# Kernel tuning notes

Hardware: AMD Instinct MI355X
Metric: run time of the kernel (lower is better)

## Reference

```python
import jax, jax.numpy as jnp
import numpy as np

N = 10000
IN_DIM = 512
OUT_DIM = 128
E = 262144


def setup_inputs() -> dict:
    key = jax.random.key(0)
    ks = jax.random.split(key, 7)
    x = jax.random.normal(ks[0], (N, IN_DIM), dtype=jnp.float32)
    adj = jax.random.uniform(ks[1], (N, N), dtype=jnp.float32) * (1.0 / N)
    # xavier-ish scaled params
    weight = jax.random.normal(ks[2], (IN_DIM, OUT_DIM), dtype=jnp.float32) * (1.0 / np.sqrt(IN_DIM))
    weight_two = jax.random.normal(ks[3], (2 * OUT_DIM, OUT_DIM), dtype=jnp.float32) * (1.0 / np.sqrt(2 * OUT_DIM))
    weight_three = jax.random.normal(ks[4], (2 * OUT_DIM, 1), dtype=jnp.float32) * (1.0 / np.sqrt(2 * OUT_DIM))
    train_edges = jax.random.randint(ks[5], (E, 2), 0, N, dtype=jnp.int32)
    train_false_edges = jax.random.randint(ks[6], (E, 2), 0, N, dtype=jnp.int32)
    return {
        "x": x,
        "adj": adj,
        "weight": weight,
        "weight_two": weight_two,
        "weight_three": weight_three,
        "train_edges": train_edges,
        "train_false_edges": train_false_edges,
    }


def reference(x, adj, weight, weight_two, weight_three, train_edges, train_false_edges):
    # encode: z = adj @ (x @ W)   -> [N, OUT_DIM]
    z = adj @ (x @ weight)
    # decode: vectorized per-edge gather of both endpoints
    edges = jnp.concatenate([train_edges, train_false_edges], axis=0)  # [2E, 2]
    zi = z[edges[:, 0]]  # [2E, OUT_DIM]
    zj = z[edges[:, 1]]  # [2E, OUT_DIM]
    z_pair = jnp.concatenate([zi, zj], axis=1)          # [2E, 2*OUT_DIM]
    z_mult = zi * zj                                     # [2E, OUT_DIM]
    z_pair = jax.nn.relu(z_pair) @ weight_two            # [2E, OUT_DIM]
    logits = jnp.concatenate([z_pair, z_mult], axis=1) @ weight_three  # [2E, 1]
    return jax.nn.sigmoid(logits)
```

## Files before the change

kernel.cpp:

```cpp
#include <hip/hip_runtime.h>

#define N_NODES 10000
#define IN_DIM  512
#define OUT_DIM 128
#define NE      262144
#define K_DIM   10000
#define HT_S    10048

#define BM 128
#define BN 128
#define BK 64
#define SPLITS 8
#define KSTEPS_TOTAL 157
#define STEPS_PER_SPLIT 20

typedef __attribute__((ext_vector_type(8))) __bf16 bf16x8;
typedef __attribute__((ext_vector_type(4))) float  f32x4;

__device__ inline ushort f2bf(float f) {
    uint u = __float_as_uint(f);
    return (ushort)((u + 0x7fffu + ((u >> 16) & 1u)) >> 16);
}
__device__ inline float bf2f(ushort s) {
    return __uint_as_float(((uint)s) << 16);
}

__device__ __forceinline__ void gl2lds16(const void* g, void* l) {
    __builtin_amdgcn_global_load_lds(
        (const __attribute__((address_space(1))) void*)g,
        (__attribute__((address_space(3))) void*)l, 16, 0, 0);
}

__global__ __launch_bounds__(256) void k_prep(const float* __restrict__ w,
                                              const float* __restrict__ w2,
                                              const float* __restrict__ w3,
                                              ushort* __restrict__ WT,
                                              float* __restrict__ v,
                                              ushort* __restrict__ hT) {
    const int t = threadIdx.x;
    for (int idx = blockIdx.x * 256 + t; idx < IN_DIM * OUT_DIM; idx += gridDim.x * 256) {
        int k = idx >> 7, n = idx & 127;
        WT[n * IN_DIM + k] = f2bf(w[idx]);
    }
    if (blockIdx.x == 0) {
        float s = 0.f;
        for (int j = 0; j < OUT_DIM; ++j) s += w2[t * OUT_DIM + j] * w3[j];
        v[t] = s;
    }
    if (blockIdx.x == 1) {
        for (int idx = t; idx < 128 * (HT_S - N_NODES); idx += 256) {
            int c = idx / (HT_S - N_NODES), r = idx % (HT_S - N_NODES);
            hT[(size_t)c * HT_S + N_NODES + r] = 0;
        }
    }
}

__global__ __launch_bounds__(64) void k_xw(const float* __restrict__ x,
                                           const ushort* __restrict__ WT,
                                           ushort* __restrict__ hT) {
    const int lane = threadIdx.x;
    const int lr = lane & 15, lg = lane >> 4;
    const int r0 = blockIdx.x * 16;
    const int c0 = blockIdx.y * 32;
    const float* pA = x + (size_t)(r0 + lr) * IN_DIM;

    f32x4 acc[2];
#pragma unroll
    for (int nf = 0; nf < 2; ++nf) acc[nf] = (f32x4){0.f, 0.f, 0.f, 0.f};

#pragma unroll
    for (int st = 0; st < 8; ++st) {
        const int k0 = st * 64;
        bf16x8 abf[2];
#pragma unroll
        for (int kh = 0; kh < 2; ++kh) {
            float4 a0 = *(const float4*)(pA + k0 + kh * 32 + lg * 8);
            float4 a1 = *(const float4*)(pA + k0 + kh * 32 + lg * 8 + 4);
            ushort* ap = (ushort*)&abf[kh];
            ap[0] = f2bf(a0.x); ap[1] = f2bf(a0.y); ap[2] = f2bf(a0.z); ap[3] = f2bf(a0.w);
            ap[4] = f2bf(a1.x); ap[5] = f2bf(a1.y); ap[6] = f2bf(a1.z); ap[7] = f2bf(a1.w);
        }
#pragma unroll
        for (int kh = 0; kh < 2; ++kh)
#pragma unroll
            for (int nf = 0; nf < 2; ++nf) {
                bf16x8 bfv = *(const bf16x8*)(WT + (size_t)(c0 + nf * 16 + lr) * IN_DIM + k0 + kh * 32 + lg * 8);
                acc[nf] = __builtin_amdgcn_mfma_f32_16x16x32_bf16(abf[kh], bfv, acc[nf], 0, 0, 0);
            }
    }

    const int m0 = r0 + lg * 4;
#pragma unroll
    for (int nf = 0; nf < 2; ++nf) {
        int c = c0 + nf * 16 + lr;
        ushort4 pk;
        pk.x = f2bf(acc[nf][0]); pk.y = f2bf(acc[nf][1]);
        pk.z = f2bf(acc[nf][2]); pk.w = f2bf(acc[nf][3]);
        *(ushort4*)(hT + (size_t)c * HT_S + m0) = pk;
    }
}

__global__ __launch_bounds__(256, 3) void k_adj(const float* __restrict__ adj,
                                                const ushort* __restrict__ hT,
                                                float* __restrict__ zp) {
    __shared__ ushort Bs[BN * BK];

    const int tid = threadIdx.x, wave = tid >> 6, lane = tid & 63;
    const int lr = lane & 15, lg = lane >> 4;
    const int m0 = blockIdx.x * BM;
    const int split = blockIdx.y;
    const int step0 = split * STEPS_PER_SPLIT;
    const int step1 = min(step0 + STEPS_PER_SPLIT, KSTEPS_TOTAL);

    long  bbase[4];
    char* bldst[4];
#pragma unroll
    for (int q = 0; q < 4; ++q) {
        int c = tid + q * 256;
        int row = c >> 3, ch = c & 7;
        bbase[q] = (long)row * HT_S + (long)((ch ^ (row & 7)) * 8);
        bldst[q] = (char*)Bs + c * 16;
    }

    const int ar0 = min(m0 + wave * 32 + lr,      N_NODES - 1);
    const int ar1 = min(m0 + wave * 32 + 16 + lr, N_NODES - 1);
    const float* pA0 = adj + (size_t)ar0 * K_DIM;
    const float* pA1 = adj + (size_t)ar1 * K_DIM;

    f32x4 acc[2][8];
#pragma unroll
    for (int mf = 0; mf < 2; ++mf)
#pragma unroll
        for (int nf = 0; nf < 8; ++nf) acc[mf][nf] = (f32x4){0.f, 0.f, 0.f, 0.f};

    const char* Bb = (const char*)Bs;

    for (int st = step0; st < step1; ++st) {
        const int k0 = st * BK;

#pragma unroll
        for (int q = 0; q < 4; ++q)
            gl2lds16(hT + (bbase[q] + k0), bldst[q]);

        float4 fa[2][2][2];
#pragma unroll
        for (int kh = 0; kh < 2; ++kh) {
            int kk = k0 + kh * 32 + lg * 8;
            int kc = (kk <= K_DIM - 8) ? kk : (K_DIM - 8);
            fa[0][kh][0] = *(const float4*)(pA0 + kc);
            fa[0][kh][1] = *(const float4*)(pA0 + kc + 4);
            fa[1][kh][0] = *(const float4*)(pA1 + kc);
            fa[1][kh][1] = *(const float4*)(pA1 + kc + 4);
        }

        __syncthreads();

        bf16x8 abf[2][2];
#pragma unroll
        for (int mf = 0; mf < 2; ++mf)
#pragma unroll
            for (int kh = 0; kh < 2; ++kh) {
                ushort* ap = (ushort*)&abf[mf][kh];
                const float* f0 = (const float*)&fa[mf][kh][0];
#pragma unroll
                for (int e = 0; e < 8; ++e) ap[e] = f2bf(f0[e]);
            }

#pragma unroll
        for (int kh = 0; kh < 2; ++kh)
#pragma unroll
            for (int nf = 0; nf < 8; ++nf) {
                int brow = nf * 16 + lr;
                bf16x8 bv = *(const bf16x8*)(Bb + brow * 128 + ((kh * 64 + lg * 16) ^ ((brow & 7) << 4)));
                acc[0][nf] = __builtin_amdgcn_mfma_f32_16x16x32_bf16(abf[0][kh], bv, acc[0][nf], 0, 0, 0);
                acc[1][nf] = __builtin_amdgcn_mfma_f32_16x16x32_bf16(abf[1][kh], bv, acc[1][nf], 0, 0, 0);
            }

        __syncthreads();
    }

    float* out = zp + (size_t)split * N_NODES * OUT_DIM;
#pragma unroll
    for (int mf = 0; mf < 2; ++mf) {
        const int orow = m0 + wave * 32 + mf * 16 + lg * 4;
#pragma unroll
        for (int nf = 0; nf < 8; ++nf)
#pragma unroll
            for (int r = 0; r < 4; ++r) {
                int row = orow + r;
                if (row < N_NODES)
                    out[(size_t)row * OUT_DIM + nf * 16 + lr] = acc[mf][nf][r];
            }
    }
}

__global__ __launch_bounds__(256) void k_node(const float* __restrict__ zp,
                                              const float* __restrict__ v,
                                              const float* __restrict__ w3,
                                              float* __restrict__ a,
                                              float* __restrict__ b,
                                              ushort* __restrict__ zb,
                                              ushort* __restrict__ zwb) {
    const int wave = threadIdx.x >> 6, lane = threadIdx.x & 63;
    const int i = blockIdx.x * 4 + wave;
    if (i >= N_NODES) return;
    const int k0 = lane, k1 = lane + 64;

    float z0 = 0.f, z1 = 0.f;
#pragma unroll
    for (int s = 0; s < SPLITS; ++s) {
        const float* row = zp + ((size_t)s * N_NODES + i) * OUT_DIM;
        z0 += row[k0];
        z1 += row[k1];
    }
    zb[(size_t)i * OUT_DIM + k0]  = f2bf(z0);
    zb[(size_t)i * OUT_DIM + k1]  = f2bf(z1);
    zwb[(size_t)i * OUT_DIM + k0] = f2bf(z0 * w3[OUT_DIM + k0]);
    zwb[(size_t)i * OUT_DIM + k1] = f2bf(z1 * w3[OUT_DIM + k1]);

    float ra = fmaxf(z0, 0.f) * v[k0] + fmaxf(z1, 0.f) * v[k1];
    float rb = fmaxf(z0, 0.f) * v[OUT_DIM + k0] + fmaxf(z1, 0.f) * v[OUT_DIM + k1];
#pragma unroll
    for (int off = 32; off; off >>= 1) {
        ra += __shfl_down(ra, off);
        rb += __shfl_down(rb, off);
    }
    if (lane == 0) { a[i] = ra; b[i] = rb; }
}

__global__ __launch_bounds__(256) void k_edge(const int* __restrict__ e_true,
                                              const int* __restrict__ e_false,
                                              const float* __restrict__ a,
                                              const float* __restrict__ b,
                                              const ushort* __restrict__ zb,
                                              const ushort* __restrict__ zwb,
                                              float* __restrict__ out) {
    const int lane = threadIdx.x & 63;
    const int half = lane >> 5, l32 = lane & 31;
    const int gw   = (blockIdx.x * blockDim.x + threadIdx.x) >> 6;
    const int nw   = (gridDim.x * blockDim.x) >> 6;

    for (int e = gw * 2 + half; e < 2 * NE; e += nw * 2) {
        int2 ij = (e < NE) ? ((const int2*)e_true)[e] : ((const int2*)e_false)[e - NE];
        int i = ij.x, j = ij.y;

        uint2 zwi = *(const uint2*)(zwb + (size_t)i * OUT_DIM + l32 * 4);
        uint2 zjv = *(const uint2*)(zb  + (size_t)j * OUT_DIM + l32 * 4);
        float d = bf2f((ushort)(zwi.x & 0xffffu)) * bf2f((ushort)(zjv.x & 0xffffu))
                + bf2f((ushort)(zwi.x >> 16))     * bf2f((ushort)(zjv.x >> 16))
                + bf2f((ushort)(zwi.y & 0xffffu)) * bf2f((ushort)(zjv.y & 0xffffu))
                + bf2f((ushort)(zwi.y >> 16))     * bf2f((ushort)(zjv.y >> 16));
#pragma unroll
        for (int off = 16; off; off >>= 1) d += __shfl_xor(d, off, 32);
        if (l32 == 0) {
            float logit = a[i] + b[j] + d;
            out[e] = 1.0f / (1.0f + __expf(-logit));
        }
    }
}

extern "C" void kernel_launch(void* const* d_in, const int* in_sizes, int n_in,
                              void* d_out, int out_size, void* d_ws, size_t ws_size,
                              hipStream_t stream) {
    const float* x      = (const float*)d_in[0];
    const float* adj    = (const float*)d_in[1];
    const float* w      = (const float*)d_in[2];
    const float* w2     = (const float*)d_in[3];
    const float* w3     = (const float*)d_in[4];
    const int* e_true   = (const int*)d_in[5];
    const int* e_false  = (const int*)d_in[6];
    float* out          = (float*)d_out;

    char* ws = (char*)d_ws;
    ushort* hT  = (ushort*)(ws);
    float*  zp  = (float*)(ws + 2572288);
    float*  v   = (float*)(ws + 43532288);
    float*  a   = (float*)(ws + 43533312);
    float*  b   = (float*)(ws + 43573312);
    ushort* zb  = (ushort*)(ws + 43613312);
    ushort* zwb = (ushort*)(ws + 46173312);
    ushort* WT  = (ushort*)(ws + 48733312);

    k_prep<<<64, 256, 0, stream>>>(w, w2, w3, WT, v, hT);
    k_xw<<<dim3(625, 4), 64, 0, stream>>>(x, WT, hT);
    k_adj<<<dim3(79, SPLITS), 256, 0, stream>>>(adj, hT, zp);
    k_node<<<2500, 256, 0, stream>>>(zp, v, w3, a, b, zb, zwb);
    k_edge<<<2048, 256, 0, stream>>>(e_true, e_false, a, b, zb, zwb, out);
}
```

Before: 208.8 us.

## Halve adj GEMM row tile, merge xw blocks, drop zwb buffer

The adjacency GEMM tile shrinks from 128 to 64 rows: each wave now handles 16 rows instead of 32, and the grid doubles to 157x8 blocks. This should raise occupancy and parallelism for the dominant memory-bound adj read, but it halves reuse of each hT tile staged in LDS. The x@W kernel is restructured so four waves in one 256-thread block cover all column groups. The precomputed z*w3 buffer is removed and the w3 scaling moves into the edge kernel, which cuts node-kernel writes but adds a multiply per element in the edge loop.

```diff
diff --git a/kernel.cpp b/kernel.cpp
--- a/kernel.cpp
+++ b/kernel.cpp
@@ -7,7 +7,7 @@
 #define K_DIM   10000
 #define HT_S    10048
 
-#define BM 128
+#define BM 64
 #define BN 128
 #define BK 64
 #define SPLITS 8
@@ -55,13 +55,13 @@
     }
 }
 
-__global__ __launch_bounds__(64) void k_xw(const float* __restrict__ x,
-                                           const ushort* __restrict__ WT,
-                                           ushort* __restrict__ hT) {
-    const int lane = threadIdx.x;
+__global__ __launch_bounds__(256) void k_xw(const float* __restrict__ x,
+                                            const ushort* __restrict__ WT,
+                                            ushort* __restrict__ hT) {
+    const int tid = threadIdx.x, wave = tid >> 6, lane = tid & 63;
     const int lr = lane & 15, lg = lane >> 4;
     const int r0 = blockIdx.x * 16;
-    const int c0 = blockIdx.y * 32;
+    const int c0 = wave * 32;
     const float* pA = x + (size_t)(r0 + lr) * IN_DIM;
 
     f32x4 acc[2];
@@ -100,9 +100,9 @@
     }
 }
 
-__global__ __launch_bounds__(256, 3) void k_adj(const float* __restrict__ adj,
-                                                const ushort* __restrict__ hT,
-                                                float* __restrict__ zp) {
+__global__ __launch_bounds__(256) void k_adj(const float* __restrict__ adj,
+                                             const ushort* __restrict__ hT,
+                                             float* __restrict__ zp) {
     __shared__ ushort Bs[BN * BK];
 
     const int tid = threadIdx.x, wave = tid >> 6, lane = tid & 63;
@@ -122,16 +122,12 @@
         bldst[q] = (char*)Bs + c * 16;
     }
 
-    const int ar0 = min(m0 + wave * 32 + lr,      N_NODES - 1);
-    const int ar1 = min(m0 + wave * 32 + 16 + lr, N_NODES - 1);
-    const float* pA0 = adj + (size_t)ar0 * K_DIM;
-    const float* pA1 = adj + (size_t)ar1 * K_DIM;
-
-    f32x4 acc[2][8];
-#pragma unroll
-    for (int mf = 0; mf < 2; ++mf)
-#pragma unroll
-        for (int nf = 0; nf < 8; ++nf) acc[mf][nf] = (f32x4){0.f, 0.f, 0.f, 0.f};
+    const int arow = min(m0 + wave * 16 + lr, N_NODES - 1);
+    const float* pA = adj + (size_t)arow * K_DIM;
+
+    f32x4 acc[8];
+#pragma unroll
+    for (int nf = 0; nf < 8; ++nf) acc[nf] = (f32x4){0.f, 0.f, 0.f, 0.f};
 
     const char* Bb = (const char*)Bs;
 
@@ -142,29 +138,25 @@
         for (int q = 0; q < 4; ++q)
             gl2lds16(hT + (bbase[q] + k0), bldst[q]);
 
-        float4 fa[2][2][2];
+        float4 fa[2][2];
 #pragma unroll
         for (int kh = 0; kh < 2; ++kh) {
             int kk = k0 + kh * 32 + lg * 8;
             int kc = (kk <= K_DIM - 8) ? kk : (K_DIM - 8);
-            fa[0][kh][0] = *(const float4*)(pA0 + kc);
-            fa[0][kh][1] = *(const float4*)(pA0 + kc + 4);
-            fa[1][kh][0] = *(const float4*)(pA1 + kc);
-            fa[1][kh][1] = *(const float4*)(pA1 + kc + 4);
+            fa[kh][0] = *(const float4*)(pA + kc);
+            fa[kh][1] = *(const float4*)(pA + kc + 4);
         }
 
         __syncthreads();
 
-        bf16x8 abf[2][2];
-#pragma unroll
-        for (int mf = 0; mf < 2; ++mf)
-#pragma unroll
-            for (int kh = 0; kh < 2; ++kh) {
-                ushort* ap = (ushort*)&abf[mf][kh];
-                const float* f0 = (const float*)&fa[mf][kh][0];
-#pragma unroll
-                for (int e = 0; e < 8; ++e) ap[e] = f2bf(f0[e]);
-            }
+        bf16x8 abf[2];
+#pragma unroll
+        for (int kh = 0; kh < 2; ++kh) {
+            ushort* ap = (ushort*)&abf[kh];
+            const float* f0 = (const float*)&fa[kh][0];
+#pragma unroll
+            for (int e = 0; e < 8; ++e) ap[e] = f2bf(f0[e]);
+        }
 
 #pragma unroll
         for (int kh = 0; kh < 2; ++kh)
@@ -172,35 +164,29 @@
             for (int nf = 0; nf < 8; ++nf) {
                 int brow = nf * 16 + lr;
                 bf16x8 bv = *(const bf16x8*)(Bb + brow * 128 + ((kh * 64 + lg * 16) ^ ((brow & 7) << 4)));
-                acc[0][nf] = __builtin_amdgcn_mfma_f32_16x16x32_bf16(abf[0][kh], bv, acc[0][nf], 0, 0, 0);
-                acc[1][nf] = __builtin_amdgcn_mfma_f32_16x16x32_bf16(abf[1][kh], bv, acc[1][nf], 0, 0, 0);
+                acc[nf] = __builtin_amdgcn_mfma_f32_16x16x32_bf16(abf[kh], bv, acc[nf], 0, 0, 0);
             }
 
         __syncthreads();
     }
 
     float* out = zp + (size_t)split * N_NODES * OUT_DIM;
-#pragma unroll
-    for (int mf = 0; mf < 2; ++mf) {
-        const int orow = m0 + wave * 32 + mf * 16 + lg * 4;
-#pragma unroll
-        for (int nf = 0; nf < 8; ++nf)
-#pragma unroll
-            for (int r = 0; r < 4; ++r) {
-                int row = orow + r;
-                if (row < N_NODES)
-                    out[(size_t)row * OUT_DIM + nf * 16 + lr] = acc[mf][nf][r];
-            }
-    }
+    const int orow = m0 + wave * 16 + lg * 4;
+#pragma unroll
+    for (int nf = 0; nf < 8; ++nf)
+#pragma unroll
+        for (int r = 0; r < 4; ++r) {
+            int row = orow + r;
+            if (row < N_NODES)
+                out[(size_t)row * OUT_DIM + nf * 16 + lr] = acc[nf][r];
+        }
 }
 
 __global__ __launch_bounds__(256) void k_node(const float* __restrict__ zp,
                                               const float* __restrict__ v,
-                                              const float* __restrict__ w3,
                                               float* __restrict__ a,
                                               float* __restrict__ b,
-                                              ushort* __restrict__ zb,
-                                              ushort* __restrict__ zwb) {
+                                              ushort* __restrict__ zb) {
     const int wave = threadIdx.x >> 6, lane = threadIdx.x & 63;
     const int i = blockIdx.x * 4 + wave;
     if (i >= N_NODES) return;
@@ -213,10 +199,8 @@
         z0 += row[k0];
         z1 += row[k1];
     }
-    zb[(size_t)i * OUT_DIM + k0]  = f2bf(z0);
-    zb[(size_t)i * OUT_DIM + k1]  = f2bf(z1);
-    zwb[(size_t)i * OUT_DIM + k0] = f2bf(z0 * w3[OUT_DIM + k0]);
-    zwb[(size_t)i * OUT_DIM + k1] = f2bf(z1 * w3[OUT_DIM + k1]);
+    zb[(size_t)i * OUT_DIM + k0] = f2bf(z0);
+    zb[(size_t)i * OUT_DIM + k1] = f2bf(z1);
 
     float ra = fmaxf(z0, 0.f) * v[k0] + fmaxf(z1, 0.f) * v[k1];
     float rb = fmaxf(z0, 0.f) * v[OUT_DIM + k0] + fmaxf(z1, 0.f) * v[OUT_DIM + k1];
@@ -233,23 +217,25 @@
                                               const float* __restrict__ a,
                                               const float* __restrict__ b,
                                               const ushort* __restrict__ zb,
-                                              const ushort* __restrict__ zwb,
+                                              const float* __restrict__ w3,
                                               float* __restrict__ out) {
     const int lane = threadIdx.x & 63;
     const int half = lane >> 5, l32 = lane & 31;
     const int gw   = (blockIdx.x * blockDim.x + threadIdx.x) >> 6;
     const int nw   = (gridDim.x * blockDim.x) >> 6;
 
+    const float4 wv = *(const float4*)(w3 + OUT_DIM + l32 * 4);
+
     for (int e = gw * 2 + half; e < 2 * NE; e += nw * 2) {
         int2 ij = (e < NE) ? ((const int2*)e_true)[e] : ((const int2*)e_false)[e - NE];
         int i = ij.x, j = ij.y;
 
-        uint2 zwi = *(const uint2*)(zwb + (size_t)i * OUT_DIM + l32 * 4);
-        uint2 zjv = *(const uint2*)(zb  + (size_t)j * OUT_DIM + l32 * 4);
-        float d = bf2f((ushort)(zwi.x & 0xffffu)) * bf2f((ushort)(zjv.x & 0xffffu))
-                + bf2f((ushort)(zwi.x >> 16))     * bf2f((ushort)(zjv.x >> 16))
-                + bf2f((ushort)(zwi.y & 0xffffu)) * bf2f((ushort)(zjv.y & 0xffffu))
-                + bf2f((ushort)(zwi.y >> 16))     * bf2f((ushort)(zjv.y >> 16));
+        uint2 zi = *(const uint2*)(zb + (size_t)i * OUT_DIM + l32 * 4);
+        uint2 zj = *(const uint2*)(zb + (size_t)j * OUT_DIM + l32 * 4);
+        float d = wv.x * bf2f((ushort)(zi.x & 0xffffu)) * bf2f((ushort)(zj.x & 0xffffu))
+                + wv.y * bf2f((ushort)(zi.x >> 16))     * bf2f((ushort)(zj.x >> 16))
+                + wv.z * bf2f((ushort)(zi.y & 0xffffu)) * bf2f((ushort)(zj.y & 0xffffu))
+                + wv.w * bf2f((ushort)(zi.y >> 16))     * bf2f((ushort)(zj.y >> 16));
 #pragma unroll
         for (int off = 16; off; off >>= 1) d += __shfl_xor(d, off, 32);
         if (l32 == 0) {
@@ -278,12 +264,11 @@
     float*  a   = (float*)(ws + 43533312);
     float*  b   = (float*)(ws + 43573312);
     ushort* zb  = (ushort*)(ws + 43613312);
-    ushort* zwb = (ushort*)(ws + 46173312);
-    ushort* WT  = (ushort*)(ws + 48733312);
+    ushort* WT  = (ushort*)(ws + 46173312);
 
     k_prep<<<64, 256, 0, stream>>>(w, w2, w3, WT, v, hT);
-    k_xw<<<dim3(625, 4), 64, 0, stream>>>(x, WT, hT);
-    k_adj<<<dim3(79, SPLITS), 256, 0, stream>>>(adj, hT, zp);
-    k_node<<<2500, 256, 0, stream>>>(zp, v, w3, a, b, zb, zwb);
-    k_edge<<<2048, 256, 0, stream>>>(e_true, e_false, a, b, zb, zwb, out);
-}
+    k_xw<<<625, 256, 0, stream>>>(x, WT, hT);
+    k_adj<<<dim3(157, SPLITS), 256, 0, stream>>>(adj, hT, zp);
+    k_node<<<2500, 256, 0, stream>>>(zp, v, a, b, zb);
+    k_edge<<<2048, 256, 0, stream>>>(e_true, e_false, a, b, zb, w3, out);
+}
```

Measured after the change: 208.1 us. Within noise of the previous version (-0.3%).
